# Kernel optimization log

Hardware: AMD Instinct MI355X
Metric: run time of the kernel (lower is better)

## Reference

```python
import jax, jax.numpy as jnp
import numpy as np

N = 2048      # nodes
E = 65536     # edges (avg degree 32)
NV = 6        # n_views (edge_attr dim)
C1, C2, C3 = 32, 32, 32


def _nnconv(x, edge_index, edge_attr, W, b, root, bias, in_c, out_c):
    # Edge MLP: Linear(n_views, in*out) + ReLU -> per-edge weight matrix [E, in, out]
    w = jax.nn.relu(edge_attr @ W + b).reshape(-1, in_c, out_c)
    src, dst = edge_index[0], edge_index[1]  # source_to_target flow
    msg = jnp.einsum('ei,eio->eo', x[src], w)          # gather + edge-specific matmul
    summed = jax.ops.segment_sum(msg, dst, num_segments=N)
    cnt = jax.ops.segment_sum(jnp.ones((msg.shape[0],), x.dtype), dst, num_segments=N)
    agg = summed / jnp.maximum(cnt, 1.0)[:, None]       # scatter-mean (0 for isolated nodes)
    return agg + x @ root + bias                        # root weight + bias (PyG NNConv defaults)


def setup_inputs() -> dict:
    key = jax.random.key(0)
    ks = jax.random.split(key, 12)
    s = 0.1
    return {
        'x': jax.random.normal(ks[0], (N, 1), jnp.float32),
        'edge_attr': jax.random.uniform(ks[1], (E, NV), jnp.float32),
        'edge_index': jax.random.randint(ks[2], (2, E), 0, N, jnp.int64),
        'W1': jax.random.normal(ks[3], (NV, 1 * C1), jnp.float32) * s,
        'b1': jnp.zeros((1 * C1,), jnp.float32),
        'root1': jax.random.normal(ks[4], (1, C1), jnp.float32) * s,
        'bias1': jnp.zeros((C1,), jnp.float32),
        'W2': jax.random.normal(ks[5], (NV, C1 * C2), jnp.float32) * s,
        'b2': jnp.zeros((C1 * C2,), jnp.float32),
        'root2': jax.random.normal(ks[6], (C1, C2), jnp.float32) * s,
        'bias2': jnp.zeros((C2,), jnp.float32),
        'W3': jax.random.normal(ks[7], (NV, C2 * C3), jnp.float32) * s,
        'b3': jnp.zeros((C2 * C3,), jnp.float32),
        'root3': jax.random.normal(ks[8], (C2, C3), jnp.float32) * s,
        'bias3': jnp.zeros((C3,), jnp.float32),
    }


def reference(x, edge_attr, edge_index, W1, b1, root1, bias1, W2, b2, root2, bias2, W3, b3, root3, bias3):
    h = jax.nn.relu(_nnconv(x, edge_index, edge_attr, W1, b1, root1, bias1, 1, C1))
    h = jax.nn.relu(_nnconv(h, edge_index, edge_attr, W2, b2, root2, bias2, C1, C2))
    h = jax.nn.relu(_nnconv(h, edge_index, edge_attr, W3, b3, root3, bias3, C2, C3))
    # CBT: cbt[i, j] = sum_k |h[j, k] - h[i, k]|  (all-pairs L1 distance, [N, N])
    cbt = jnp.sum(jnp.abs(h[None, :, :] - h[:, None, :]), axis=2)
    return cbt
```

## Files before the change

### kernel.cpp

```cpp
#include <hip/hip_runtime.h>

#define N_NODES 2048
#define N_EDGES 65536
#define NV 6
#define C 32
#define BLK 256


__global__ void edge1_kernel(const float* __restrict__ x,
                             const float* __restrict__ ea,
                             const int* __restrict__ src,
                             const int* __restrict__ dst,
                             const float* __restrict__ W1,
                             const float* __restrict__ b1,
                             float* __restrict__ sum1,
                             float* __restrict__ sum23,
                             float* __restrict__ cnt) {
    int t = blockIdx.x * blockDim.x + threadIdx.x;
    if (t < 2 * N_NODES * C) sum23[t] = 0.0f;
    int e = t >> 5, o = t & 31;
    if (e >= N_EDGES) return;
    const float* eap = ea + e * NV;
    float w = b1[o];
#pragma unroll
    for (int v = 0; v < NV; v++) w = fmaf(eap[v], W1[v * C + o], w);
    w = fmaxf(w, 0.0f);
    int d = dst[e];
    atomicAdd(&sum1[d * C + o], x[src[e]] * w);
    if (o == 0) atomicAdd(&cnt[d], 1.0f);
}

template <int IN_C>
__global__ void node_kernel(const float* __restrict__ sum,
                            const float* __restrict__ cnt,
                            const float* __restrict__ hprev,
                            const float* __restrict__ root,
                            const float* __restrict__ bias,
                            float* __restrict__ hout) {
    int t = blockIdx.x * blockDim.x + threadIdx.x;
    int n = t >> 5, o = t & 31;
    float inv = 1.0f / fmaxf(cnt[n], 1.0f);
    float acc = sum[t] * inv + bias[o];
    if constexpr (IN_C == 1) {
        acc = fmaf(hprev[n], root[o], acc);
    } else {
        const float4* hp4 = (const float4*)(hprev + n * IN_C);
#pragma unroll
        for (int q = 0; q < IN_C / 4; q++) {
            float4 hv = hp4[q];
            acc = fmaf(hv.x, root[(q * 4 + 0) * C + o], acc);
            acc = fmaf(hv.y, root[(q * 4 + 1) * C + o], acc);
            acc = fmaf(hv.z, root[(q * 4 + 2) * C + o], acc);
            acc = fmaf(hv.w, root[(q * 4 + 3) * C + o], acc);
        }
    }
    hout[t] = fmaxf(acc, 0.0f);
}

__global__ __launch_bounds__(BLK, 2) void edge23_kernel(
    const float* __restrict__ hprev,
    const float* __restrict__ ea,
    const int* __restrict__ src,
    const int* __restrict__ dst,
    const float* __restrict__ W,
    const float* __restrict__ b,
    float* __restrict__ sumout)
{
    __shared__ float hb[4][4][256];
    const int lane = threadIdx.x & 63;
    const int o = lane & 31;
    const int half = lane >> 5;
    const int i0 = half * 16;
    const int w = threadIdx.x >> 6;

    float wreg[16][6], breg[16];
#pragma unroll
    for (int j = 0; j < 16; j++) {
#pragma unroll
        for (int v = 0; v < 6; v++) wreg[j][v] = W[v * 1024 + (i0 + j) * C + o];
        breg[j] = b[(i0 + j) * C + o];
    }

    const int wid = (blockIdx.x * BLK + threadIdx.x) >> 6;

    int4 sqs[4];
#pragma unroll
    for (int i = 0; i < 4; i++)
        sqs[i] = *(const int4*)&src[(wid + i * 2048) * 8 + half * 4];
#pragma unroll
    for (int i = 0; i < 4; i++) {
        float4 hq;
        hq.x = hprev[sqs[i].x * C + o];
        hq.y = hprev[sqs[i].y * C + o];
        hq.z = hprev[sqs[i].z * C + o];
        hq.w = hprev[sqs[i].w * C + o];
        *(float4*)&hb[w][i][half * 128 + o * 4] = hq;
    }

#pragma unroll 2
    for (int i = 0; i < 4; i++) {
        const int e0 = (wid + i * 2048) * 8;
        const float* hbw = &hb[w][i][0];
        const float4* eap4 = (const float4*)(ea + (size_t)e0 * NV);
        float accs[8];
#pragma unroll
        for (int sub = 0; sub < 2; sub++) {
            float eaf[24];
#pragma unroll
            for (int t = 0; t < 6; t++) *(float4*)&eaf[t * 4] = eap4[sub * 6 + t];
            float a0 = 0.0f, a1 = 0.0f, a2 = 0.0f, a3 = 0.0f;
#pragma unroll
            for (int j = 0; j < 16; j++) {
                const float4 hA = *(const float4*)&hbw[sub * 128 + (i0 + j) * 4];
                const float bb = breg[j];
                const float w0 = wreg[j][0], w1 = wreg[j][1], w2 = wreg[j][2];
                const float w3 = wreg[j][3], w4 = wreg[j][4], w5 = wreg[j][5];
                float t0 = bb, t1 = bb, t2 = bb, t3 = bb;
                t0 = fmaf(eaf[0],  w0, t0); t1 = fmaf(eaf[6],  w0, t1);
                t2 = fmaf(eaf[12], w0, t2); t3 = fmaf(eaf[18], w0, t3);
                t0 = fmaf(eaf[1],  w1, t0); t1 = fmaf(eaf[7],  w1, t1);
                t2 = fmaf(eaf[13], w1, t2); t3 = fmaf(eaf[19], w1, t3);
                t0 = fmaf(eaf[2],  w2, t0); t1 = fmaf(eaf[8],  w2, t1);
                t2 = fmaf(eaf[14], w2, t2); t3 = fmaf(eaf[20], w2, t3);
                t0 = fmaf(eaf[3],  w3, t0); t1 = fmaf(eaf[9],  w3, t1);
                t2 = fmaf(eaf[15], w3, t2); t3 = fmaf(eaf[21], w3, t3);
                t0 = fmaf(eaf[4],  w4, t0); t1 = fmaf(eaf[10], w4, t1);
                t2 = fmaf(eaf[16], w4, t2); t3 = fmaf(eaf[22], w4, t3);
                t0 = fmaf(eaf[5],  w5, t0); t1 = fmaf(eaf[11], w5, t1);
                t2 = fmaf(eaf[17], w5, t2); t3 = fmaf(eaf[23], w5, t3);
                a0 = fmaf(hA.x, fmaxf(t0, 0.0f), a0);
                a1 = fmaf(hA.y, fmaxf(t1, 0.0f), a1);
                a2 = fmaf(hA.z, fmaxf(t2, 0.0f), a2);
                a3 = fmaf(hA.w, fmaxf(t3, 0.0f), a3);
            }
            accs[sub * 4 + 0] = a0; accs[sub * 4 + 1] = a1;
            accs[sub * 4 + 2] = a2; accs[sub * 4 + 3] = a3;
        }
#pragma unroll
        for (int k = 0; k < 8; k++) accs[k] += __shfl_down(accs[k], 32);

        const int4 dA = *(const int4*)&dst[e0];
        const int4 dB = *(const int4*)&dst[e0 + 4];
        if (lane < 32) {
            atomicAdd(&sumout[dA.x * C + o], accs[0]);
            atomicAdd(&sumout[dA.y * C + o], accs[1]);
            atomicAdd(&sumout[dA.z * C + o], accs[2]);
            atomicAdd(&sumout[dA.w * C + o], accs[3]);
            atomicAdd(&sumout[dB.x * C + o], accs[4]);
            atomicAdd(&sumout[dB.y * C + o], accs[5]);
            atomicAdd(&sumout[dB.z * C + o], accs[6]);
            atomicAdd(&sumout[dB.w * C + o], accs[7]);
        }
    }
}

__global__ __launch_bounds__(BLK) void cbt_kernel(const float* __restrict__ h,
                                                  float* __restrict__ out) {
    const int bx = blockIdx.x, by = blockIdx.y;
    if (by > bx) return;
    __shared__ float hj_s[64][33];
    __shared__ float hi_s[64 * 32];
    __shared__ float tile[64][65];
    const int lane = threadIdx.x & 63;
    const int w = threadIdx.x >> 6;
    const int j0 = bx * 64;
    const int i0 = by * 64;
    for (int t = threadIdx.x; t < 64 * 32; t += BLK) {
        hj_s[t >> 5][t & 31] = h[j0 * 32 + t];
        hi_s[t] = h[i0 * 32 + t];
    }
    __syncthreads();
    float hj[32];
#pragma unroll
    for (int k = 0; k < 32; k++) hj[k] = hj_s[lane][k];
    const int j = j0 + lane;
#pragma unroll 4
    for (int ii = w * 16; ii < w * 16 + 16; ii++) {
        float acc = 0.0f;
#pragma unroll
        for (int k = 0; k < 32; k++) acc += fabsf(hi_s[ii * 32 + k] - hj[k]);
        out[(size_t)(i0 + ii) * N_NODES + j] = acc;
        tile[ii][lane] = acc;
    }
    if (by == bx) return;
    __syncthreads();
#pragma unroll 4
    for (int k = 0; k < 16; k++) {
        const int jj = w * 16 + k;
        out[(size_t)(j0 + jj) * N_NODES + i0 + lane] = tile[lane][jj];
    }
}

extern "C" void kernel_launch(void* const* d_in, const int* in_sizes, int n_in,
                              void* d_out, int out_size, void* d_ws, size_t ws_size,
                              hipStream_t stream) {
    const float* x         = (const float*)d_in[0];
    const float* edge_attr = (const float*)d_in[1];
    const int*   edge_idx  = (const int*)d_in[2];
    const float* W1 = (const float*)d_in[3];
    const float* b1 = (const float*)d_in[4];
    const float* root1 = (const float*)d_in[5];
    const float* bias1 = (const float*)d_in[6];
    const float* W2 = (const float*)d_in[7];
    const float* b2 = (const float*)d_in[8];
    const float* root2 = (const float*)d_in[9];
    const float* bias2 = (const float*)d_in[10];
    const float* W3 = (const float*)d_in[11];
    const float* b3 = (const float*)d_in[12];
    const float* root3 = (const float*)d_in[13];
    const float* bias3 = (const float*)d_in[14];

    const int* src = edge_idx;
    const int* dst = edge_idx + N_EDGES;

    float* ws   = (float*)d_ws;
    float* cnt  = ws;
    float* sum1 = ws + N_NODES;
    float* sum2 = sum1 + N_NODES * C;
    float* sum3 = sum2 + N_NODES * C;
    float* h1   = sum3 + N_NODES * C;
    float* h2   = h1 + N_NODES * C;
    float* h3   = h2 + N_NODES * C;

    hipMemsetAsync(d_ws, 0, (size_t)(N_NODES + N_NODES * C) * sizeof(float), stream);

    edge1_kernel<<<(N_EDGES * C) / BLK, BLK, 0, stream>>>(x, edge_attr, src, dst,
                                                          W1, b1, sum1, sum2, cnt);
    node_kernel<1><<<(N_NODES * C) / BLK, BLK, 0, stream>>>(sum1, cnt, x, root1, bias1, h1);

    edge23_kernel<<<512, BLK, 0, stream>>>(h1, edge_attr, src, dst, W2, b2, sum2);
    node_kernel<C><<<(N_NODES * C) / BLK, BLK, 0, stream>>>(sum2, cnt, h1, root2, bias2, h2);

    edge23_kernel<<<512, BLK, 0, stream>>>(h2, edge_attr, src, dst, W3, b3, sum3);
    node_kernel<C><<<(N_NODES * C) / BLK, BLK, 0, stream>>>(sum3, cnt, h2, root3, bias3, h3);

    cbt_kernel<<<dim3(N_NODES / 64, N_NODES / 64), BLK, 0, stream>>>(h3, (float*)d_out);
}
```

Baseline: 167.0 us.

## Fuse final node update into CBT kernel and launch only triangular tiles

Removes the third node_kernel launch by recomputing each tile's h3 rows (mean aggregation, root matmul, bias, ReLU) inside the CBT kernel while it loads its tiles. The 2D grid with half the blocks exiting early becomes a 1D grid of 528 blocks that covers only the upper triangle, with the tile coordinates recovered through a sqrt-based index. This saves one launch and the h3 round-trip through memory. In exchange, every block redundantly computes 128 node rows with a 32-wide root matmul, which adds arithmetic and global reads of h2 and root3.

```diff
diff --git a/kernel.cpp b/kernel.cpp
--- a/kernel.cpp
+++ b/kernel.cpp
@@ -154,10 +154,18 @@
     }
 }
 
-__global__ __launch_bounds__(BLK) void cbt_kernel(const float* __restrict__ h,
+__global__ __launch_bounds__(BLK) void cbt_kernel(const float* __restrict__ sum3,
+                                                  const float* __restrict__ cnt,
+                                                  const float* __restrict__ h2,
+                                                  const float* __restrict__ root3,
+                                                  const float* __restrict__ bias3,
                                                   float* __restrict__ out) {
-    const int bx = blockIdx.x, by = blockIdx.y;
-    if (by > bx) return;
+    const int L = blockIdx.x;
+    int bx = (int)((sqrtf(8.0f * L + 1.0f) - 1.0f) * 0.5f);
+    while ((bx + 1) * (bx + 2) / 2 <= L) bx++;
+    while (bx * (bx + 1) / 2 > L) bx--;
+    const int by = L - bx * (bx + 1) / 2;
+
     __shared__ float hj_s[64][33];
     __shared__ float hi_s[64 * 32];
     __shared__ float tile[64][65];
@@ -165,11 +173,44 @@
     const int w = threadIdx.x >> 6;
     const int j0 = bx * 64;
     const int i0 = by * 64;
-    for (int t = threadIdx.x; t < 64 * 32; t += BLK) {
-        hj_s[t >> 5][t & 31] = h[j0 * 32 + t];
-        hi_s[t] = h[i0 * 32 + t];
+
+#pragma unroll
+    for (int r = 0; r < 8; r++) {
+        const int elem = threadIdx.x + r * 256;
+        const int n = elem >> 5, o = elem & 31;
+        {
+            const int ng = j0 + n;
+            const float inv = 1.0f / fmaxf(cnt[ng], 1.0f);
+            float acc = sum3[ng * 32 + o] * inv + bias3[o];
+            const float4* hp4 = (const float4*)(h2 + ng * 32);
+#pragma unroll
+            for (int q = 0; q < 8; q++) {
+                float4 hv = hp4[q];
+                acc = fmaf(hv.x, root3[(q * 4 + 0) * 32 + o], acc);
+                acc = fmaf(hv.y, root3[(q * 4 + 1) * 32 + o], acc);
+                acc = fmaf(hv.z, root3[(q * 4 + 2) * 32 + o], acc);
+                acc = fmaf(hv.w, root3[(q * 4 + 3) * 32 + o], acc);
+            }
+            hj_s[n][o] = fmaxf(acc, 0.0f);
+        }
+        {
+            const int ng = i0 + n;
+            const float inv = 1.0f / fmaxf(cnt[ng], 1.0f);
+            float acc = sum3[ng * 32 + o] * inv + bias3[o];
+            const float4* hp4 = (const float4*)(h2 + ng * 32);
+#pragma unroll
+            for (int q = 0; q < 8; q++) {
+                float4 hv = hp4[q];
+                acc = fmaf(hv.x, root3[(q * 4 + 0) * 32 + o], acc);
+                acc = fmaf(hv.y, root3[(q * 4 + 1) * 32 + o], acc);
+                acc = fmaf(hv.z, root3[(q * 4 + 2) * 32 + o], acc);
+                acc = fmaf(hv.w, root3[(q * 4 + 3) * 32 + o], acc);
+            }
+            hi_s[n * 32 + o] = fmaxf(acc, 0.0f);
+        }
     }
     __syncthreads();
+
     float hj[32];
 #pragma unroll
     for (int k = 0; k < 32; k++) hj[k] = hj_s[lane][k];
@@ -220,7 +261,6 @@
     float* sum3 = sum2 + N_NODES * C;
     float* h1   = sum3 + N_NODES * C;
     float* h2   = h1 + N_NODES * C;
-    float* h3   = h2 + N_NODES * C;
 
     hipMemsetAsync(d_ws, 0, (size_t)(N_NODES + N_NODES * C) * sizeof(float), stream);
 
@@ -232,7 +272,6 @@
     node_kernel<C><<<(N_NODES * C) / BLK, BLK, 0, stream>>>(sum2, cnt, h1, root2, bias2, h2);
 
     edge23_kernel<<<512, BLK, 0, stream>>>(h2, edge_attr, src, dst, W3, b3, sum3);
-    node_kernel<C><<<(N_NODES * C) / BLK, BLK, 0, stream>>>(sum3, cnt, h2, root3, bias3, h3);
-
-    cbt_kernel<<<dim3(N_NODES / 64, N_NODES / 64), BLK, 0, stream>>>(h3, (float*)d_out);
-}
+
+    cbt_kernel<<<528, BLK, 0, stream>>>(sum3, cnt, h2, root3, bias3, (float*)d_out);
+}
```

Result: slower. 179.1 us (+7.2%).
